# Optimization experiments

Hardware: AMD Instinct MI355X
Metric: run time of the kernel (lower is better)

The kernel has to match this reference:

```python
import jax, jax.numpy as jnp
import numpy as np

B_SZ, C_IN, C_OUT, H, W = 16, 32, 32, 128, 128
K, CODE, PAD, FACTOR = 3, 2, 1, 1.0

def setup_inputs() -> dict:
    key = jax.random.key(0)
    ks = jax.random.split(key, 7)
    s = 0.05
    return {
        "x": jax.random.normal(ks[0], (B_SZ, C_IN, H, W), jnp.float32),
        "codes": jax.random.normal(ks[1], (B_SZ, CODE, CODE), jnp.float32),
        "weight": jax.random.normal(ks[2], (C_OUT, C_IN, K, K), jnp.float32) * s,
        "A": jax.random.normal(ks[3], (C_IN, CODE, K, K), jnp.float32) * s,
        "Bm": jax.random.normal(ks[4], (C_OUT, CODE, K, K), jnp.float32) * s,
        "bias": jax.random.normal(ks[5], (C_OUT,), jnp.float32) * s,
        "bias_context": jax.random.normal(ks[6], (CODE, C_OUT), jnp.float32) * s,
    }

def reference(x, codes, weight, A, Bm, bias, bias_context):
    # hypernetwork weight synthesis: [b, out, in, k, k]
    w_ctx = jnp.einsum('ickl,bcr->birkl', A, codes)            # [b, in, code, k, k]
    w_ctx = jnp.einsum('birkl,orkl->boikl', w_ctx, Bm)         # [b, out, in, k, k]
    combined_weight = weight[None] + FACTOR * w_ctx
    # per-sample bias from diagonal of codes
    diag = jnp.diagonal(codes, axis1=-2, axis2=-1)             # [b, code]
    combined_bias = bias[None] + FACTOR * (diag @ bias_context)  # [b, out]
    # circular padding then per-sample VALID conv (== unfold + einsum)
    xp = jnp.pad(x, ((0, 0), (0, 0), (PAD, PAD), (PAD, PAD)), mode='wrap')
    def conv_one(xi, wi):
        return jax.lax.conv_general_dilated(
            xi[None], wi, window_strides=(1, 1), padding='VALID',
            dimension_numbers=('NCHW', 'OIHW', 'NCHW'))[0]
    out = jax.vmap(conv_one)(xp, combined_weight)              # [b, out, H, W]
    return out + combined_bias[:, :, None, None]
```

## Files before the change

### kernel.cpp

```cpp
#include <hip/hip_runtime.h>

typedef short bf16x8 __attribute__((ext_vector_type(8)));
typedef float f32x4  __attribute__((ext_vector_type(4)));
typedef unsigned short u16;
typedef unsigned int   u32;

#define HH 128
#define WW 128

__device__ __forceinline__ u32 cvt_pk_bf16(float lo, float hi) {
    u32 r;
    asm volatile("v_cvt_pk_bf16_f32 %0, %1, %2" : "=v"(r) : "v"(lo), "v"(hi));
    return r;
}

__global__ __launch_bounds__(1024, 1) void geps_mfma_kernel(
    const float* __restrict__ x, const float* __restrict__ codes,
    const float* __restrict__ weight, const float* __restrict__ A,
    const float* __restrict__ Bm, const float* __restrict__ bias,
    const float* __restrict__ bctx, float* __restrict__ out)
{
    __shared__ bf16x8 lds_x[5120];
    __shared__ bf16x8 lds_w[1152];
    __shared__ float  lds_ctx[576];
    __shared__ float  lds_b[32];

    const int tid  = threadIdx.x;
    const int l    = tid & 63;
    const int wvid = tid >> 6;
    const int row  = wvid >> 1;
    const int nh   = wvid & 1;

    const int orig = blockIdx.x;
    const int vb   = (orig & 7) * 32 + (orig >> 3);
    const int b    = vb >> 4;
    const int grp  = vb & 15;
    const int h0   = grp * 8;

    const float c00 = codes[b * 4 + 0];
    const float c01 = codes[b * 4 + 1];
    const float c10 = codes[b * 4 + 2];
    const float c11 = codes[b * 4 + 3];

    if (tid < 576) {
        int j = tid;
        int i = j / 18, rem = j % 18, r = rem / 9, kl = rem % 9;
        float a0 = A[(i * 2 + 0) * 9 + kl];
        float a1 = A[(i * 2 + 1) * 9 + kl];
        lds_ctx[j] = (r == 0) ? (a0 * c00 + a1 * c10) : (a0 * c01 + a1 * c11);
    }
    if (tid < 32) lds_b[tid] = bias[tid] + c00 * bctx[tid] + c11 * bctx[32 + tid];
    __syncthreads();

    #pragma unroll
    for (int it = 0; it < 5; ++it) {
        int idx   = it * 1024 + tid;
        int jh    = idx & 1;
        int cp    = (idx >> 1) & 63;
        int ig    = (idx >> 7) & 3;
        int rr    = idx >> 9;
        int c0    = cp * 2;
        int grow  = (h0 - 1 + rr) & 127;
        const float* src =
            x + ((size_t)(b * 32 + ig * 8 + jh * 4) * HH + grow) * WW + c0;
        float2 f[4];
        #pragma unroll
        for (int jj = 0; jj < 4; ++jj)
            f[jj] = *(const float2*)(src + (size_t)jj * HH * WW);
        u32 w0a = cvt_pk_bf16(f[0].x, f[1].x);
        u32 w0b = cvt_pk_bf16(f[2].x, f[3].x);
        u32 w1a = cvt_pk_bf16(f[0].y, f[1].y);
        u32 w1b = cvt_pk_bf16(f[2].y, f[3].y);
        int didx = rr * 512 + (c0 >> 4) * 64 + ig * 16 + (c0 & 15);
        u32* base = (u32*)lds_x;
        *(uint2*)&base[didx * 4 + jh * 2]       = make_uint2(w0a, w0b);
        *(uint2*)&base[(didx + 1) * 4 + jh * 2] = make_uint2(w1a, w1b);
    }

    for (int j = tid; j < 1152; j += 1024) {
        int kl = j >> 7, rem = j & 127, o = rem >> 2, kb = rem & 3;
        float m0 = Bm[(o * 2 + 0) * 9 + kl];
        float m1 = Bm[(o * 2 + 1) * 9 + kl];
        float wf[8];
        #pragma unroll
        for (int jj = 0; jj < 8; ++jj) {
            int i = kb * 8 + jj;
            wf[jj] = weight[(o * 32 + i) * 9 + kl]
                   + lds_ctx[i * 18 + kl] * m0
                   + lds_ctx[i * 18 + 9 + kl] * m1;
        }
        u32 pk[4];
        #pragma unroll
        for (int q = 0; q < 4; ++q) pk[q] = cvt_pk_bf16(wf[2 * q], wf[2 * q + 1]);
        *(uint4*)&lds_w[kl * 128 + (o >> 4) * 64 + kb * 16 + (o & 15)] =
            make_uint4(pk[0], pk[1], pk[2], pk[3]);
    }
    __syncthreads();

    const int awb = (l >> 4) * 16 + (l & 15);
    bf16x8 af0[9];
    #pragma unroll
    for (int kl = 0; kl < 9; ++kl)
        af0[kl] = lds_w[kl * 128 + awb];

    const int p = l & 15, igf = l >> 4;
    int bb[3];
    #pragma unroll
    for (int dl = -1; dl <= 1; ++dl) {
        int pq = p + dl;
        bb[dl + 1] = (pq & 15) + ((pq >> 4) << 6) + igf * 16;
    }

    f32x4 acc[2][4];
    #pragma unroll
    for (int oh = 0; oh < 2; ++oh)
        #pragma unroll
        for (int q = 0; q < 4; ++q) acc[oh][q] = (f32x4){0.f, 0.f, 0.f, 0.f};

    #pragma unroll
    for (int lc = 0; lc < 3; ++lc) {
        #pragma unroll
        for (int k = 0; k < 3; ++k) {
            const bf16x8 a0 = af0[k * 3 + lc];
            const bf16x8 a1 = lds_w[(k * 3 + lc) * 128 + 64 + awb];
            #pragma unroll
            for (int q = 0; q < 4; ++q) {
                int t = (bb[lc] + (nh * 4 + q) * 64) & 511;
                bf16x8 bfv = lds_x[(row + k) * 512 + t];
                acc[0][q] = __builtin_amdgcn_mfma_f32_16x16x32_bf16(
                    a0, bfv, acc[0][q], 0, 0, 0);
                acc[1][q] = __builtin_amdgcn_mfma_f32_16x16x32_bf16(
                    a1, bfv, acc[1][q], 0, 0, 0);
            }
        }
    }

    float blr[2][4];
    #pragma unroll
    for (int oh = 0; oh < 2; ++oh)
        #pragma unroll
        for (int r = 0; r < 4; ++r)
            blr[oh][r] = lds_b[oh * 16 + (l >> 4) * 4 + r];

    const int h = h0 + row;
    const size_t obase = ((size_t)(b * 32 + (l >> 4) * 4) * HH + h) * WW + p;
    #pragma unroll
    for (int oh = 0; oh < 2; ++oh)
        #pragma unroll
        for (int q = 0; q < 4; ++q)
            #pragma unroll
            for (int r = 0; r < 4; ++r)
                out[obase + (size_t)(oh * 16 + r) * (HH * WW) + (nh * 4 + q) * 16] =
                    acc[oh][q][r] + blr[oh][r];
}

extern "C" void kernel_launch(void* const* d_in, const int* in_sizes, int n_in,
                              void* d_out, int out_size, void* d_ws, size_t ws_size,
                              hipStream_t stream) {
    const float* x      = (const float*)d_in[0];
    const float* codes  = (const float*)d_in[1];
    const float* weight = (const float*)d_in[2];
    const float* A      = (const float*)d_in[3];
    const float* Bm     = (const float*)d_in[4];
    const float* bias   = (const float*)d_in[5];
    const float* bctx   = (const float*)d_in[6];
    float* out = (float*)d_out;

    hipLaunchKernelGGL(geps_mfma_kernel, dim3(256), dim3(1024), 0, stream,
                       x, codes, weight, A, Bm, bias, bctx, out);
}
```

Measured before the change: 23.73 us.

## Split conv into two row phases overlapping halo loads with compute and specialize weight-synthesis wave

Dedicates one wave to building the synthesized weights and bias while the other fifteen waves load the first six input rows into LDS. The remaining four rows are prefetched into registers and written to LDS after the first half of the output rows is computed, so their global latency overlaps MFMA work. The wave-to-work mapping changes from 8 rows by 2 column halves to 4 rows by 4 column quarters, processed in two passes. This adds a second barrier and more register pressure from the prefetched values, and the single synthesis wave could become the critical path.

```diff
diff --git a/kernel.cpp b/kernel.cpp
--- a/kernel.cpp
+++ b/kernel.cpp
@@ -28,8 +28,6 @@
     const int tid  = threadIdx.x;
     const int l    = tid & 63;
     const int wvid = tid >> 6;
-    const int row  = wvid >> 1;
-    const int nh   = wvid & 1;
 
     const int orig = blockIdx.x;
     const int vb   = (orig & 7) * 32 + (orig >> 3);
@@ -37,67 +35,94 @@
     const int grp  = vb & 15;
     const int h0   = grp * 8;
 
-    const float c00 = codes[b * 4 + 0];
-    const float c01 = codes[b * 4 + 1];
-    const float c10 = codes[b * 4 + 2];
-    const float c11 = codes[b * 4 + 3];
-
-    if (tid < 576) {
-        int j = tid;
-        int i = j / 18, rem = j % 18, r = rem / 9, kl = rem % 9;
-        float a0 = A[(i * 2 + 0) * 9 + kl];
-        float a1 = A[(i * 2 + 1) * 9 + kl];
-        lds_ctx[j] = (r == 0) ? (a0 * c00 + a1 * c10) : (a0 * c01 + a1 * c11);
-    }
-    if (tid < 32) lds_b[tid] = bias[tid] + c00 * bctx[tid] + c11 * bctx[32 + tid];
+    u32* const xb32 = (u32*)lds_x;
+
+    if (wvid == 15) {
+        const float c00 = codes[b * 4 + 0];
+        const float c01 = codes[b * 4 + 1];
+        const float c10 = codes[b * 4 + 2];
+        const float c11 = codes[b * 4 + 3];
+        #pragma unroll
+        for (int q = 0; q < 9; ++q) {
+            int j = q * 64 + l;
+            int i = j / 18, rem = j % 18, r = rem / 9, kl = rem % 9;
+            float a0 = A[(i * 2 + 0) * 9 + kl];
+            float a1 = A[(i * 2 + 1) * 9 + kl];
+            lds_ctx[j] = (r == 0) ? (a0 * c00 + a1 * c10) : (a0 * c01 + a1 * c11);
+        }
+        for (int q = 0; q < 18; ++q) {
+            int j = q * 64 + l;
+            int kl = j >> 7, rem = j & 127, o = rem >> 2, kb = rem & 3;
+            float m0 = Bm[(o * 2 + 0) * 9 + kl];
+            float m1 = Bm[(o * 2 + 1) * 9 + kl];
+            float wf[8];
+            #pragma unroll
+            for (int jj = 0; jj < 8; ++jj) {
+                int i = kb * 8 + jj;
+                wf[jj] = weight[(o * 32 + i) * 9 + kl]
+                       + lds_ctx[i * 18 + kl] * m0
+                       + lds_ctx[i * 18 + 9 + kl] * m1;
+            }
+            u32 pk[4];
+            #pragma unroll
+            for (int qq = 0; qq < 4; ++qq)
+                pk[qq] = cvt_pk_bf16(wf[2 * qq], wf[2 * qq + 1]);
+            *(uint4*)&lds_w[kl * 128 + (o >> 4) * 64 + kb * 16 + (o & 15)] =
+                make_uint4(pk[0], pk[1], pk[2], pk[3]);
+        }
+        if (l < 32)
+            lds_b[l] = bias[l] + c00 * bctx[l] + c11 * bctx[32 + l];
+    } else {
+        #pragma unroll
+        for (int it = 0; it < 4; ++it) {
+            int idx = it * 960 + tid;
+            if (idx < 3072) {
+                int jh = idx & 1;
+                int cp = (idx >> 1) & 63;
+                int ig = (idx >> 7) & 3;
+                int rr = idx >> 9;
+                int c0 = cp * 2;
+                int grow = (h0 - 1 + rr) & 127;
+                const float* src =
+                    x + ((size_t)(b * 32 + ig * 8 + jh * 4) * HH + grow) * WW + c0;
+                float2 f[4];
+                #pragma unroll
+                for (int jj = 0; jj < 4; ++jj)
+                    f[jj] = *(const float2*)(src + (size_t)jj * HH * WW);
+                u32 w0a = cvt_pk_bf16(f[0].x, f[1].x);
+                u32 w0b = cvt_pk_bf16(f[2].x, f[3].x);
+                u32 w1a = cvt_pk_bf16(f[0].y, f[1].y);
+                u32 w1b = cvt_pk_bf16(f[2].y, f[3].y);
+                int didx = rr * 512 + (c0 >> 4) * 64 + ig * 16 + (c0 & 15);
+                *(uint2*)&xb32[didx * 4 + jh * 2]       = make_uint2(w0a, w0b);
+                *(uint2*)&xb32[(didx + 1) * 4 + jh * 2] = make_uint2(w1a, w1b);
+            }
+        }
+    }
     __syncthreads();
 
-    #pragma unroll
-    for (int it = 0; it < 5; ++it) {
-        int idx   = it * 1024 + tid;
-        int jh    = idx & 1;
-        int cp    = (idx >> 1) & 63;
-        int ig    = (idx >> 7) & 3;
-        int rr    = idx >> 9;
-        int c0    = cp * 2;
-        int grow  = (h0 - 1 + rr) & 127;
+    float2 pf[2][4];
+    int pidx[2];
+    #pragma unroll
+    for (int it = 0; it < 2; ++it) {
+        int idx = it * 1024 + tid;
+        pidx[it] = idx;
+        int jh = idx & 1;
+        int cp = (idx >> 1) & 63;
+        int ig = (idx >> 7) & 3;
+        int rr = 6 + (idx >> 9);
+        int grow = (h0 - 1 + rr) & 127;
         const float* src =
-            x + ((size_t)(b * 32 + ig * 8 + jh * 4) * HH + grow) * WW + c0;
-        float2 f[4];
+            x + ((size_t)(b * 32 + ig * 8 + jh * 4) * HH + grow) * WW + cp * 2;
         #pragma unroll
         for (int jj = 0; jj < 4; ++jj)
-            f[jj] = *(const float2*)(src + (size_t)jj * HH * WW);
-        u32 w0a = cvt_pk_bf16(f[0].x, f[1].x);
-        u32 w0b = cvt_pk_bf16(f[2].x, f[3].x);
-        u32 w1a = cvt_pk_bf16(f[0].y, f[1].y);
-        u32 w1b = cvt_pk_bf16(f[2].y, f[3].y);
-        int didx = rr * 512 + (c0 >> 4) * 64 + ig * 16 + (c0 & 15);
-        u32* base = (u32*)lds_x;
-        *(uint2*)&base[didx * 4 + jh * 2]       = make_uint2(w0a, w0b);
-        *(uint2*)&base[(didx + 1) * 4 + jh * 2] = make_uint2(w1a, w1b);
-    }
-
-    for (int j = tid; j < 1152; j += 1024) {
-        int kl = j >> 7, rem = j & 127, o = rem >> 2, kb = rem & 3;
-        float m0 = Bm[(o * 2 + 0) * 9 + kl];
-        float m1 = Bm[(o * 2 + 1) * 9 + kl];
-        float wf[8];
-        #pragma unroll
-        for (int jj = 0; jj < 8; ++jj) {
-            int i = kb * 8 + jj;
-            wf[jj] = weight[(o * 32 + i) * 9 + kl]
-                   + lds_ctx[i * 18 + kl] * m0
-                   + lds_ctx[i * 18 + 9 + kl] * m1;
-        }
-        u32 pk[4];
-        #pragma unroll
-        for (int q = 0; q < 4; ++q) pk[q] = cvt_pk_bf16(wf[2 * q], wf[2 * q + 1]);
-        *(uint4*)&lds_w[kl * 128 + (o >> 4) * 64 + kb * 16 + (o & 15)] =
-            make_uint4(pk[0], pk[1], pk[2], pk[3]);
-    }
-    __syncthreads();
-
+            pf[it][jj] = *(const float2*)(src + (size_t)jj * HH * WW);
+    }
+
+    const int row = wvid >> 2;
+    const int nq  = wvid & 3;
     const int awb = (l >> 4) * 16 + (l & 15);
+
     bf16x8 af0[9];
     #pragma unroll
     for (int kl = 0; kl < 9; ++kl)
@@ -111,30 +136,6 @@
         bb[dl + 1] = (pq & 15) + ((pq >> 4) << 6) + igf * 16;
     }
 
-    f32x4 acc[2][4];
-    #pragma unroll
-    for (int oh = 0; oh < 2; ++oh)
-        #pragma unroll
-        for (int q = 0; q < 4; ++q) acc[oh][q] = (f32x4){0.f, 0.f, 0.f, 0.f};
-
-    #pragma unroll
-    for (int lc = 0; lc < 3; ++lc) {
-        #pragma unroll
-        for (int k = 0; k < 3; ++k) {
-            const bf16x8 a0 = af0[k * 3 + lc];
-            const bf16x8 a1 = lds_w[(k * 3 + lc) * 128 + 64 + awb];
-            #pragma unroll
-            for (int q = 0; q < 4; ++q) {
-                int t = (bb[lc] + (nh * 4 + q) * 64) & 511;
-                bf16x8 bfv = lds_x[(row + k) * 512 + t];
-                acc[0][q] = __builtin_amdgcn_mfma_f32_16x16x32_bf16(
-                    a0, bfv, acc[0][q], 0, 0, 0);
-                acc[1][q] = __builtin_amdgcn_mfma_f32_16x16x32_bf16(
-                    a1, bfv, acc[1][q], 0, 0, 0);
-            }
-        }
-    }
-
     float blr[2][4];
     #pragma unroll
     for (int oh = 0; oh < 2; ++oh)
@@ -142,16 +143,61 @@
         for (int r = 0; r < 4; ++r)
             blr[oh][r] = lds_b[oh * 16 + (l >> 4) * 4 + r];
 
-    const int h = h0 + row;
-    const size_t obase = ((size_t)(b * 32 + (l >> 4) * 4) * HH + h) * WW + p;
-    #pragma unroll
-    for (int oh = 0; oh < 2; ++oh)
-        #pragma unroll
-        for (int q = 0; q < 4; ++q)
-            #pragma unroll
-            for (int r = 0; r < 4; ++r)
-                out[obase + (size_t)(oh * 16 + r) * (HH * WW) + (nh * 4 + q) * 16] =
-                    acc[oh][q][r] + blr[oh][r];
+    auto compute_store = [&](int s, int h) {
+        f32x4 acc[2][2];
+        #pragma unroll
+        for (int oh = 0; oh < 2; ++oh)
+            #pragma unroll
+            for (int q = 0; q < 2; ++q) acc[oh][q] = (f32x4){0.f, 0.f, 0.f, 0.f};
+        #pragma unroll
+        for (int lc = 0; lc < 3; ++lc) {
+            #pragma unroll
+            for (int k = 0; k < 3; ++k) {
+                const bf16x8 a0 = af0[k * 3 + lc];
+                const bf16x8 a1 = lds_w[(k * 3 + lc) * 128 + 64 + awb];
+                #pragma unroll
+                for (int q = 0; q < 2; ++q) {
+                    int t = (bb[lc] + (nq * 2 + q) * 64) & 511;
+                    bf16x8 bfv = lds_x[(s + k) * 512 + t];
+                    acc[0][q] = __builtin_amdgcn_mfma_f32_16x16x32_bf16(
+                        a0, bfv, acc[0][q], 0, 0, 0);
+                    acc[1][q] = __builtin_amdgcn_mfma_f32_16x16x32_bf16(
+                        a1, bfv, acc[1][q], 0, 0, 0);
+                }
+            }
+        }
+        const size_t obase = ((size_t)(b * 32 + (l >> 4) * 4) * HH + h) * WW + p;
+        #pragma unroll
+        for (int oh = 0; oh < 2; ++oh)
+            #pragma unroll
+            for (int q = 0; q < 2; ++q)
+                #pragma unroll
+                for (int r = 0; r < 4; ++r)
+                    out[obase + (size_t)(oh * 16 + r) * (HH * WW) +
+                        (nq * 2 + q) * 16] = acc[oh][q][r] + blr[oh][r];
+    };
+
+    compute_store(row, h0 + row);
+
+    #pragma unroll
+    for (int it = 0; it < 2; ++it) {
+        int idx = pidx[it];
+        int jh = idx & 1;
+        int cp = (idx >> 1) & 63;
+        int ig = (idx >> 7) & 3;
+        int rr = 6 + (idx >> 9);
+        int c0 = cp * 2;
+        u32 w0a = cvt_pk_bf16(pf[it][0].x, pf[it][1].x);
+        u32 w0b = cvt_pk_bf16(pf[it][2].x, pf[it][3].x);
+        u32 w1a = cvt_pk_bf16(pf[it][0].y, pf[it][1].y);
+        u32 w1b = cvt_pk_bf16(pf[it][2].y, pf[it][3].y);
+        int didx = rr * 512 + (c0 >> 4) * 64 + ig * 16 + (c0 & 15);
+        *(uint2*)&xb32[didx * 4 + jh * 2]       = make_uint2(w0a, w0b);
+        *(uint2*)&xb32[(didx + 1) * 4 + jh * 2] = make_uint2(w1a, w1b);
+    }
+    __syncthreads();
+
+    compute_store(4 + row, h0 + 4 + row);
 }
 
 extern "C" void kernel_launch(void* const* d_in, const int* in_sizes, int n_in,
```

Measured after the change: 24.27 us. 2.3% more time.

## Split weight synthesis into prep kernel and use smaller conv blocks

Applied to the files above, without the earlier changes.

Per-sample combined weights and bias are now computed once per batch in a separate prep kernel and written to workspace, instead of being recomputed redundantly by every conv block. The conv kernel shrinks from 1024-thread blocks covering 8 rows to 256-thread blocks covering 2 rows, with 1024 blocks and up to 3 blocks per CU, which is meant to improve occupancy and latency hiding. The cost is an extra kernel launch, a global round-trip for the weights, and a larger halo overhead since each block now loads 4 input rows to produce 2 output rows.

```diff
diff --git a/kernel.cpp b/kernel.cpp
--- a/kernel.cpp
+++ b/kernel.cpp
@@ -2,8 +2,7 @@
 
 typedef short bf16x8 __attribute__((ext_vector_type(8)));
 typedef float f32x4  __attribute__((ext_vector_type(4)));
-typedef unsigned short u16;
-typedef unsigned int   u32;
+typedef unsigned int u32;
 
 #define HH 128
 #define WW 128
@@ -14,70 +13,28 @@
     return r;
 }
 
-__global__ __launch_bounds__(1024, 1) void geps_mfma_kernel(
-    const float* __restrict__ x, const float* __restrict__ codes,
-    const float* __restrict__ weight, const float* __restrict__ A,
-    const float* __restrict__ Bm, const float* __restrict__ bias,
-    const float* __restrict__ bctx, float* __restrict__ out)
+__global__ __launch_bounds__(256) void geps_prep_kernel(
+    const float* __restrict__ codes, const float* __restrict__ weight,
+    const float* __restrict__ A, const float* __restrict__ Bm,
+    const float* __restrict__ bias, const float* __restrict__ bctx,
+    bf16x8* __restrict__ wsw, float* __restrict__ wsb)
 {
-    __shared__ bf16x8 lds_x[5120];
-    __shared__ bf16x8 lds_w[1152];
-    __shared__ float  lds_ctx[576];
-    __shared__ float  lds_b[32];
-
-    const int tid  = threadIdx.x;
-    const int l    = tid & 63;
-    const int wvid = tid >> 6;
-    const int row  = wvid >> 1;
-    const int nh   = wvid & 1;
-
-    const int orig = blockIdx.x;
-    const int vb   = (orig & 7) * 32 + (orig >> 3);
-    const int b    = vb >> 4;
-    const int grp  = vb & 15;
-    const int h0   = grp * 8;
-
+    __shared__ float lds_ctx[576];
+    const int tid = threadIdx.x, b = blockIdx.x;
     const float c00 = codes[b * 4 + 0];
     const float c01 = codes[b * 4 + 1];
     const float c10 = codes[b * 4 + 2];
     const float c11 = codes[b * 4 + 3];
 
-    if (tid < 576) {
-        int j = tid;
+    for (int j = tid; j < 576; j += 256) {
         int i = j / 18, rem = j % 18, r = rem / 9, kl = rem % 9;
         float a0 = A[(i * 2 + 0) * 9 + kl];
         float a1 = A[(i * 2 + 1) * 9 + kl];
         lds_ctx[j] = (r == 0) ? (a0 * c00 + a1 * c10) : (a0 * c01 + a1 * c11);
     }
-    if (tid < 32) lds_b[tid] = bias[tid] + c00 * bctx[tid] + c11 * bctx[32 + tid];
     __syncthreads();
 
-    #pragma unroll
-    for (int it = 0; it < 5; ++it) {
-        int idx   = it * 1024 + tid;
-        int jh    = idx & 1;
-        int cp    = (idx >> 1) & 63;
-        int ig    = (idx >> 7) & 3;
-        int rr    = idx >> 9;
-        int c0    = cp * 2;
-        int grow  = (h0 - 1 + rr) & 127;
-        const float* src =
-            x + ((size_t)(b * 32 + ig * 8 + jh * 4) * HH + grow) * WW + c0;
-        float2 f[4];
-        #pragma unroll
-        for (int jj = 0; jj < 4; ++jj)
-            f[jj] = *(const float2*)(src + (size_t)jj * HH * WW);
-        u32 w0a = cvt_pk_bf16(f[0].x, f[1].x);
-        u32 w0b = cvt_pk_bf16(f[2].x, f[3].x);
-        u32 w1a = cvt_pk_bf16(f[0].y, f[1].y);
-        u32 w1b = cvt_pk_bf16(f[2].y, f[3].y);
-        int didx = rr * 512 + (c0 >> 4) * 64 + ig * 16 + (c0 & 15);
-        u32* base = (u32*)lds_x;
-        *(uint2*)&base[didx * 4 + jh * 2]       = make_uint2(w0a, w0b);
-        *(uint2*)&base[(didx + 1) * 4 + jh * 2] = make_uint2(w1a, w1b);
-    }
-
-    for (int j = tid; j < 1152; j += 1024) {
+    for (int j = tid; j < 1152; j += 256) {
         int kl = j >> 7, rem = j & 127, o = rem >> 2, kb = rem & 3;
         float m0 = Bm[(o * 2 + 0) * 9 + kl];
         float m1 = Bm[(o * 2 + 1) * 9 + kl];
@@ -92,16 +49,69 @@
         u32 pk[4];
         #pragma unroll
         for (int q = 0; q < 4; ++q) pk[q] = cvt_pk_bf16(wf[2 * q], wf[2 * q + 1]);
-        *(uint4*)&lds_w[kl * 128 + (o >> 4) * 64 + kb * 16 + (o & 15)] =
+        *(uint4*)&wsw[b * 1152 + kl * 128 + (o >> 4) * 64 + kb * 16 + (o & 15)] =
             make_uint4(pk[0], pk[1], pk[2], pk[3]);
     }
-    __syncthreads();
+    if (tid < 32)
+        wsb[b * 32 + tid] = bias[tid] + c00 * bctx[tid] + c11 * bctx[32 + tid];
+}
+
+__global__ __launch_bounds__(256, 3) void geps_conv_kernel(
+    const float* __restrict__ x, const bf16x8* __restrict__ wsw,
+    const float* __restrict__ wsb, float* __restrict__ out)
+{
+    __shared__ bf16x8 lds_x[2048];
+
+    const int tid = threadIdx.x;
+    const int l   = tid & 63;
+    const int wvid = tid >> 6;
+    const int row = wvid >> 1;
+    const int nh  = wvid & 1;
+
+    const int orig = blockIdx.x;
+    const int vb   = (orig & 7) * 128 + (orig >> 3);
+    const int b    = vb >> 6;
+    const int grp  = vb & 63;
+    const int h0   = grp * 2;
+
+    #pragma unroll
+    for (int it = 0; it < 4; ++it) {
+        int idx = it * 256 + tid;
+        int cp  = idx & 63;
+        int ig  = (idx >> 6) & 3;
+        int rr  = idx >> 8;
+        int c0  = cp * 2;
+        int grow = (h0 - 1 + rr) & 127;
+        const float* src = x + ((size_t)(b * 32 + ig * 8) * HH + grow) * WW + c0;
+        float2 f[8];
+        #pragma unroll
+        for (int jj = 0; jj < 8; ++jj)
+            f[jj] = *(const float2*)(src + (size_t)jj * HH * WW);
+        u32 p0[4], p1[4];
+        #pragma unroll
+        for (int q = 0; q < 4; ++q) {
+            p0[q] = cvt_pk_bf16(f[2 * q].x, f[2 * q + 1].x);
+            p1[q] = cvt_pk_bf16(f[2 * q].y, f[2 * q + 1].y);
+        }
+        int didx = rr * 512 + (c0 >> 4) * 64 + ig * 16 + (c0 & 15);
+        *(uint4*)&lds_x[didx]     = make_uint4(p0[0], p0[1], p0[2], p0[3]);
+        *(uint4*)&lds_x[didx + 1] = make_uint4(p1[0], p1[1], p1[2], p1[3]);
+    }
 
     const int awb = (l >> 4) * 16 + (l & 15);
-    bf16x8 af0[9];
+    bf16x8 af[9][2];
     #pragma unroll
     for (int kl = 0; kl < 9; ++kl)
-        af0[kl] = lds_w[kl * 128 + awb];
+        #pragma unroll
+        for (int oh = 0; oh < 2; ++oh)
+            af[kl][oh] = wsw[b * 1152 + kl * 128 + oh * 64 + awb];
+
+    float blr[2][4];
+    #pragma unroll
+    for (int oh = 0; oh < 2; ++oh)
+        #pragma unroll
+        for (int r = 0; r < 4; ++r)
+            blr[oh][r] = wsb[b * 32 + oh * 16 + (l >> 4) * 4 + r];
 
     const int p = l & 15, igf = l >> 4;
     int bb[3];
@@ -110,6 +120,8 @@
         int pq = p + dl;
         bb[dl + 1] = (pq & 15) + ((pq >> 4) << 6) + igf * 16;
     }
+
+    __syncthreads();
 
     f32x4 acc[2][4];
     #pragma unroll
@@ -121,8 +133,8 @@
     for (int lc = 0; lc < 3; ++lc) {
         #pragma unroll
         for (int k = 0; k < 3; ++k) {
-            const bf16x8 a0 = af0[k * 3 + lc];
-            const bf16x8 a1 = lds_w[(k * 3 + lc) * 128 + 64 + awb];
+            const bf16x8 a0 = af[k * 3 + lc][0];
+            const bf16x8 a1 = af[k * 3 + lc][1];
             #pragma unroll
             for (int q = 0; q < 4; ++q) {
                 int t = (bb[lc] + (nh * 4 + q) * 64) & 511;
@@ -134,13 +146,6 @@
             }
         }
     }
-
-    float blr[2][4];
-    #pragma unroll
-    for (int oh = 0; oh < 2; ++oh)
-        #pragma unroll
-        for (int r = 0; r < 4; ++r)
-            blr[oh][r] = lds_b[oh * 16 + (l >> 4) * 4 + r];
 
     const int h = h0 + row;
     const size_t obase = ((size_t)(b * 32 + (l >> 4) * 4) * HH + h) * WW + p;
@@ -166,6 +171,11 @@
     const float* bctx   = (const float*)d_in[6];
     float* out = (float*)d_out;
 
-    hipLaunchKernelGGL(geps_mfma_kernel, dim3(256), dim3(1024), 0, stream,
-                       x, codes, weight, A, Bm, bias, bctx, out);
+    bf16x8* wsw = (bf16x8*)d_ws;
+    float*  wsb = (float*)((char*)d_ws + 16 * 1152 * 16);
+
+    hipLaunchKernelGGL(geps_prep_kernel, dim3(16), dim3(256), 0, stream,
+                       codes, weight, A, Bm, bias, bctx, wsw, wsb);
+    hipLaunchKernelGGL(geps_conv_kernel, dim3(1024), dim3(256), 0, stream,
+                       x, wsw, wsb, out);
 }
```

Result: slower. 29.40 us (+23.9%).

## Prefetch x early, stage output through LDS for coalesced nontemporal stores

Applied to the files above, without the earlier changes.

Global loads of the x tile are issued at kernel start into registers, before the codes/context computation, so their latency overlaps the weight synthesis. Output is bounced through LDS with a rotated column swizzle and written as 16-byte nontemporal row-contiguous stores instead of scattered 4-byte stores. Both A-fragment halves are preloaded into registers, and __syncthreads is replaced by a lightweight lgkmcnt-wait barrier. The cost is higher register pressure from holding 40 float2 values, plus extra LDS round trips and barriers in the epilogue.

```diff
diff --git a/kernel.cpp b/kernel.cpp
--- a/kernel.cpp
+++ b/kernel.cpp
@@ -2,8 +2,7 @@
 
 typedef short bf16x8 __attribute__((ext_vector_type(8)));
 typedef float f32x4  __attribute__((ext_vector_type(4)));
-typedef unsigned short u16;
-typedef unsigned int   u32;
+typedef unsigned int u32;
 
 #define HH 128
 #define WW 128
@@ -12,6 +11,12 @@
     u32 r;
     asm volatile("v_cvt_pk_bf16_f32 %0, %1, %2" : "=v"(r) : "v"(lo), "v"(hi));
     return r;
+}
+
+__device__ __forceinline__ void lds_barrier() {
+    asm volatile("s_waitcnt lgkmcnt(0)" ::: "memory");
+    __builtin_amdgcn_s_barrier();
+    __builtin_amdgcn_sched_barrier(0);
 }
 
 __global__ __launch_bounds__(1024, 1) void geps_mfma_kernel(
@@ -37,11 +42,23 @@
     const int grp  = vb & 15;
     const int h0   = grp * 8;
 
+    float2 f[5][4];
+    #pragma unroll
+    for (int it = 0; it < 5; ++it) {
+        int idx = it * 1024 + tid;
+        int cp = idx & 63, jh = (idx >> 6) & 1, ig = (idx >> 7) & 3, rr = idx >> 9;
+        int grow = (h0 - 1 + rr) & 127;
+        const float* src =
+            x + ((size_t)(b * 32 + ig * 8 + jh * 4) * HH + grow) * WW + cp * 2;
+        #pragma unroll
+        for (int jj = 0; jj < 4; ++jj)
+            f[it][jj] = *(const float2*)(src + (size_t)jj * HH * WW);
+    }
+
     const float c00 = codes[b * 4 + 0];
     const float c01 = codes[b * 4 + 1];
     const float c10 = codes[b * 4 + 2];
     const float c11 = codes[b * 4 + 3];
-
     if (tid < 576) {
         int j = tid;
         int i = j / 18, rem = j % 18, r = rem / 9, kl = rem % 9;
@@ -50,32 +67,7 @@
         lds_ctx[j] = (r == 0) ? (a0 * c00 + a1 * c10) : (a0 * c01 + a1 * c11);
     }
     if (tid < 32) lds_b[tid] = bias[tid] + c00 * bctx[tid] + c11 * bctx[32 + tid];
-    __syncthreads();
-
-    #pragma unroll
-    for (int it = 0; it < 5; ++it) {
-        int idx   = it * 1024 + tid;
-        int jh    = idx & 1;
-        int cp    = (idx >> 1) & 63;
-        int ig    = (idx >> 7) & 3;
-        int rr    = idx >> 9;
-        int c0    = cp * 2;
-        int grow  = (h0 - 1 + rr) & 127;
-        const float* src =
-            x + ((size_t)(b * 32 + ig * 8 + jh * 4) * HH + grow) * WW + c0;
-        float2 f[4];
-        #pragma unroll
-        for (int jj = 0; jj < 4; ++jj)
-            f[jj] = *(const float2*)(src + (size_t)jj * HH * WW);
-        u32 w0a = cvt_pk_bf16(f[0].x, f[1].x);
-        u32 w0b = cvt_pk_bf16(f[2].x, f[3].x);
-        u32 w1a = cvt_pk_bf16(f[0].y, f[1].y);
-        u32 w1b = cvt_pk_bf16(f[2].y, f[3].y);
-        int didx = rr * 512 + (c0 >> 4) * 64 + ig * 16 + (c0 & 15);
-        u32* base = (u32*)lds_x;
-        *(uint2*)&base[didx * 4 + jh * 2]       = make_uint2(w0a, w0b);
-        *(uint2*)&base[(didx + 1) * 4 + jh * 2] = make_uint2(w1a, w1b);
-    }
+    lds_barrier();
 
     for (int j = tid; j < 1152; j += 1024) {
         int kl = j >> 7, rem = j & 127, o = rem >> 2, kb = rem & 3;
@@ -95,13 +87,31 @@
         *(uint4*)&lds_w[kl * 128 + (o >> 4) * 64 + kb * 16 + (o & 15)] =
             make_uint4(pk[0], pk[1], pk[2], pk[3]);
     }
-    __syncthreads();
+
+    #pragma unroll
+    for (int it = 0; it < 5; ++it) {
+        int idx = it * 1024 + tid;
+        int cp = idx & 63, jh = (idx >> 6) & 1, ig = (idx >> 7) & 3, rr = idx >> 9;
+        int c0 = cp * 2;
+        u32 a0 = cvt_pk_bf16(f[it][0].x, f[it][1].x);
+        u32 a1 = cvt_pk_bf16(f[it][2].x, f[it][3].x);
+        u32 b0 = cvt_pk_bf16(f[it][0].y, f[it][1].y);
+        u32 b1 = cvt_pk_bf16(f[it][2].y, f[it][3].y);
+        int didx = (c0 >> 4) * 64 + ig * 16 + (c0 & 15);
+        *(uint2*)((char*)lds_x + rr * 8192 + didx * 16 + jh * 8) =
+            make_uint2(a0, a1);
+        *(uint2*)((char*)lds_x + rr * 8192 + (didx + 1) * 16 + jh * 8) =
+            make_uint2(b0, b1);
+    }
+    lds_barrier();
 
     const int awb = (l >> 4) * 16 + (l & 15);
-    bf16x8 af0[9];
+    bf16x8 af[9][2];
     #pragma unroll
     for (int kl = 0; kl < 9; ++kl)
-        af0[kl] = lds_w[kl * 128 + awb];
+        #pragma unroll
+        for (int oh = 0; oh < 2; ++oh)
+            af[kl][oh] = lds_w[kl * 128 + oh * 64 + awb];
 
     const int p = l & 15, igf = l >> 4;
     int bb[3];
@@ -110,6 +120,13 @@
         int pq = p + dl;
         bb[dl + 1] = (pq & 15) + ((pq >> 4) << 6) + igf * 16;
     }
+
+    float blr[2][4];
+    #pragma unroll
+    for (int oh = 0; oh < 2; ++oh)
+        #pragma unroll
+        for (int r = 0; r < 4; ++r)
+            blr[oh][r] = lds_b[oh * 16 + (l >> 4) * 4 + r];
 
     f32x4 acc[2][4];
     #pragma unroll
@@ -121,8 +138,8 @@
     for (int lc = 0; lc < 3; ++lc) {
         #pragma unroll
         for (int k = 0; k < 3; ++k) {
-            const bf16x8 a0 = af0[k * 3 + lc];
-            const bf16x8 a1 = lds_w[(k * 3 + lc) * 128 + 64 + awb];
+            const bf16x8 a0 = af[k * 3 + lc][0];
+            const bf16x8 a1 = af[k * 3 + lc][1];
             #pragma unroll
             for (int q = 0; q < 4; ++q) {
                 int t = (bb[lc] + (nh * 4 + q) * 64) & 511;
@@ -135,23 +152,32 @@
         }
     }
 
-    float blr[2][4];
+    float* bounce = (float*)lds_x;
     #pragma unroll
-    for (int oh = 0; oh < 2; ++oh)
-        #pragma unroll
-        for (int r = 0; r < 4; ++r)
-            blr[oh][r] = lds_b[oh * 16 + (l >> 4) * 4 + r];
-
-    const int h = h0 + row;
-    const size_t obase = ((size_t)(b * 32 + (l >> 4) * 4) * HH + h) * WW + p;
-    #pragma unroll
-    for (int oh = 0; oh < 2; ++oh)
+    for (int oh = 0; oh < 2; ++oh) {
+        lds_barrier();
         #pragma unroll
         for (int q = 0; q < 4; ++q)
             #pragma unroll
-            for (int r = 0; r < 4; ++r)
-                out[obase + (size_t)(oh * 16 + r) * (HH * WW) + (nh * 4 + q) * 16] =
-                    acc[oh][q][r] + blr[oh][r];
+            for (int r = 0; r < 4; ++r) {
+                int o16  = (l >> 4) * 4 + r;
+                int col  = (nh * 4 + q) * 16 + (l & 15);
+                int col2 = (col + o16 * 4) & 127;
+                bounce[(o16 * 8 + row) * 128 + col2] = acc[oh][q][r] + blr[oh][r];
+            }
+        lds_barrier();
+        const int ch = oh * 16 + wvid;
+        #pragma unroll
+        for (int k = 0; k < 4; ++k) {
+            int hrow = 2 * k + (l >> 5);
+            int lcol = (l & 31) * 4;
+            int pcol = (lcol + wvid * 4) & 127;
+            f32x4 v = *(const f32x4*)&bounce[(wvid * 8 + hrow) * 128 + pcol];
+            __builtin_nontemporal_store(
+                v, (f32x4*)&out[((size_t)(b * 32 + ch) * HH + (h0 + hrow)) * WW +
+                                lcol]);
+        }
+    }
 }
 
 extern "C" void kernel_launch(void* const* d_in, const int* in_sizes, int n_in,
```

Result: faster. 21.40 us (-9.8%).
